# Optimization experiments

Measured on AMD Instinct MI355X. Metric: run time of the kernel, lower is better.

The kernel has to match this reference:

```python
import jax, jax.numpy as jnp
import numpy as np

EPS = 1e-6


def _ring_view(t, start, length, M):
    # contiguous logical view of `length` oldest positions starting at start
    if start + length <= M:
        return t[:, start:start + length]
    first = t[:, start:]
    return jnp.concatenate([first, t[:, :length - first.shape[1]]], axis=1)


def _ring_write(t, start, chunk, M):
    # write chunk at logical position `start`, wrapping around the ring
    C = chunk.shape[1]
    if start + C <= M:
        return t.at[:, start:start + C].set(chunk)
    first = M - start
    t = t.at[:, start:].set(chunk[:, :first])
    return t.at[:, :C - first].set(chunk[:, first:])


def setup_inputs() -> dict:
    key = jax.random.key(0)
    ks = jax.random.split(key, 9)
    B, M, Hh, D, F, C = 4, 1088, 32, 128, 128, 512
    f = lambda k, s: jax.random.normal(k, s, dtype=jnp.float32)
    return {
        "K": f(ks[0], (B, M, Hh, D)),
        "V": f(ks[1], (B, M, Hh, D)),
        "FK": f(ks[2], (B, M, Hh, F)),
        "H": f(ks[3], (B, Hh, F, D)),
        "S": f(ks[4], (B, Hh, F)),
        "k_c": f(ks[5], (B, C, Hh, D)),
        "v_c": f(ks[6], (B, C, Hh, D)),
        "fk_c": f(ks[7], (B, C, Hh, F)),
        "fq": f(ks[8], (B, C, Hh, F)),
        "write_ptr": 100,
        "valid": 1088,
    }


def reference(K, V, FK, H, S, k_c, v_c, fk_c, fq, write_ptr, valid):
    M = K.shape[1]
    C = k_c.shape[1]
    if valid + C <= M:
        # room left in ring buffer: plain write, no eviction
        pos = (write_ptr + valid) % M
        K = _ring_write(K, pos, k_c, M)
        V = _ring_write(V, pos, v_c, M)
        FK = _ring_write(FK, pos, fk_c, M)
    else:
        # evict num_excess oldest tokens into recurrent state H, S
        num_excess = valid + C - M
        old_fk = _ring_view(FK, write_ptr, num_excess, M)  # (B, E, H, F)
        old_v = _ring_view(V, write_ptr, num_excess, M)    # (B, E, H, D)
        H = H + jnp.einsum('behf,behd->bhfd', old_fk, old_v)
        S = S + old_fk.sum(axis=1)
        write_ptr = (write_ptr + num_excess) % M
        pos = (write_ptr + M) % M  # valid == M now
        K = _ring_write(K, pos, k_c, M)
        V = _ring_write(V, pos, v_c, M)
        FK = _ring_write(FK, pos, fk_c, M)
    # linear_attn_forward(fq)
    y_num = jnp.einsum('bchf,bhfd->bchd', fq, H)
    y_den = jnp.einsum('bchf,bhf->bch', fq, S)[..., None]
    return y_num, y_den, K, V, FK, H, S
```

## Files before the change

### kernel.cpp

```cpp
#include <hip/hip_runtime.h>

typedef float f32x4 __attribute__((ext_vector_type(4)));

constexpr int B  = 4;
constexpr int M  = 1088;
constexpr int HH = 32;
constexpr int D  = 128;
constexpr int F  = 128;
constexpr int C  = 512;

constexpr int SZ_YNUM = B * C * HH * D;
constexpr int SZ_YDEN = B * C * HH;
constexpr int SZ_KVM  = B * M * HH * D;
constexpr int SZ_H    = B * HH * F * D;

constexpr int OFF_YNUM = 0;
constexpr int OFF_YDEN = OFF_YNUM + SZ_YNUM;
constexpr int OFF_K    = OFF_YDEN + SZ_YDEN;
constexpr int OFF_V    = OFF_K + SZ_KVM;
constexpr int OFF_FK   = OFF_V + SZ_KVM;
constexpr int OFF_H    = OFF_FK + SZ_KVM;
constexpr int OFF_S    = OFF_H + SZ_H;

constexpr int INNER4      = HH * D / 4;
constexpr int ROWS_PER_CB = 4;
constexpr int COPY_BLOCKS = B * M / ROWS_PER_CB;
constexpr int HS_BLOCKS   = B * HH * 2;
constexpr int Y_BLOCKS    = B * HH * 8;
constexpr int ESTEP       = 16;

__device__ __forceinline__ void ring_params(const int* wp_p, const int* valid_p,
                                            int& wp, int& num_excess, int& pos) {
    wp = *wp_p;
    int valid = *valid_p;
    if (valid + C <= M) {
        num_excess = 0;
        pos = (wp + valid) % M;
    } else {
        num_excess = valid + C - M;
        pos = (wp + num_excess) % M;
    }
}

__device__ __forceinline__ void ring_copy_block(int cb, int tid,
                                                const f32x4* __restrict__ src,
                                                const f32x4* __restrict__ chk,
                                                f32x4* __restrict__ dst,
                                                int pos) {
    int bm0 = cb * ROWS_PER_CB;
#pragma unroll
    for (int r = 0; r < ROWS_PER_CB; ++r) {
        int bm = bm0 + r;
        int m = bm % M;
        int b = bm / M;
        int off = m - pos;
        if (off < 0) off += M;
        const f32x4* s = (off < C) ? &chk[(b * C + off) * INNER4]
                                   : &src[bm * INNER4];
        f32x4* d = &dst[bm * INNER4];
#pragma unroll
        for (int k = 0; k < INNER4 / 256; ++k)
            d[k * 256 + tid] = s[k * 256 + tid];
    }
}

__device__ void update_hs_body(int bx,
                               const float* __restrict__ FKi,
                               const float* __restrict__ Vi,
                               const float* __restrict__ Hi,
                               const float* __restrict__ Si,
                               float* __restrict__ Ho,
                               float* __restrict__ So,
                               int wp, int num_excess) {
    const int tid = threadIdx.x;
    const int fhalf = bx & 1;
    const int bh = bx >> 1;
    const int h = bh & (HH - 1);
    const int b = bh >> 5;
    const int fbase = fhalf * 64;

    __shared__ float  fk_s[ESTEP][64];
    __shared__ f32x4  v_s[ESTEP][32];
    __shared__ float  sred[4][64];

    const int tf = tid >> 5;
    const int td = tid & 31;
    const int cq = tid & 63;
    const int qq = tid >> 6;

    f32x4 acc[8];
#pragma unroll
    for (int i = 0; i < 8; ++i) acc[i] = (f32x4)0.f;
    float s_part = 0.f;

    float fkA[4], fkB[4];
    f32x4 vA[2],  vB[2];

    auto load_tile = [&](int e0, float* fk_r, f32x4* v_r) {
#pragma unroll
        for (int j = 0; j < 4; ++j) {
            int e = e0 + qq + 4 * j;
            int me = wp + e;
            if (me >= M) me -= M;
            if (me >= M) me -= M;
            float v = 0.f;
            if (e < num_excess) v = FKi[((b * M + me) * HH + h) * F + fbase + cq];
            fk_r[j] = v;
        }
#pragma unroll
        for (int j = 0; j < 2; ++j) {
            int e = e0 + tf + 8 * j;
            int me = wp + e;
            if (me >= M) me -= M;
            if (me >= M) me -= M;
            f32x4 v = (f32x4)0.f;
            if (e < num_excess) v = *(const f32x4*)&Vi[((b * M + me) * HH + h) * D + td * 4];
            v_r[j] = v;
        }
    };
    auto store_tile = [&](const float* fk_r, const f32x4* v_r) {
#pragma unroll
        for (int j = 0; j < 4; ++j) fk_s[qq + 4 * j][cq] = fk_r[j];
#pragma unroll
        for (int j = 0; j < 2; ++j) v_s[tf + 8 * j][td] = v_r[j];
    };
    auto compute = [&]() {
#pragma unroll
        for (int ee = 0; ee < ESTEP; ++ee) {
            f32x4 fa = *(const f32x4*)&fk_s[ee][tf * 8];
            f32x4 fb = *(const f32x4*)&fk_s[ee][tf * 8 + 4];
            f32x4 vv = v_s[ee][td];
            acc[0] += fa.x * vv; acc[1] += fa.y * vv;
            acc[2] += fa.z * vv; acc[3] += fa.w * vv;
            acc[4] += fb.x * vv; acc[5] += fb.y * vv;
            acc[6] += fb.z * vv; acc[7] += fb.w * vv;
        }
#pragma unroll
        for (int j = 0; j < 4; ++j) s_part += fk_s[qq * 4 + j][cq];
    };

    if (num_excess > 0) {
        const int nt = (num_excess + ESTEP - 1) / ESTEP;
        load_tile(0, fkA, vA);
        if (nt > 1) load_tile(ESTEP, fkB, vB);
        store_tile(fkA, vA);
        for (int t = 0; t < nt; t += 2) {
            __syncthreads();
            if (t + 2 < nt) load_tile((t + 2) * ESTEP, fkA, vA);
            compute();
            __syncthreads();
            if (t + 1 >= nt) break;
            store_tile(fkB, vB);
            __syncthreads();
            if (t + 3 < nt) load_tile((t + 3) * ESTEP, fkB, vB);
            compute();
            __syncthreads();
            if (t + 2 >= nt) break;
            store_tile(fkA, vA);
        }
    }

    sred[qq][cq] = s_part;
    __syncthreads();
    if (tid < 64) {
        int f = fbase + tid;
        int si = (b * HH + h) * F + f;
        So[si] = Si[si] + sred[0][tid] + sred[1][tid] + sred[2][tid] + sred[3][tid];
    }

#pragma unroll
    for (int i = 0; i < 8; ++i) {
        int f = fbase + tf * 8 + i;
        int base = ((b * HH + h) * F + f) * D + td * 4;
        f32x4 hold = *(const f32x4*)&Hi[base];
        *(f32x4*)&Ho[base] = hold + acc[i];
    }
}

__device__ void compute_y_den_body(int bx,
                                   const float* __restrict__ fq,
                                   const float* __restrict__ Hn,
                                   const float* __restrict__ Sn,
                                   float* __restrict__ ynum,
                                   float* __restrict__ yden) {
    const int tid = threadIdx.x;
    int t0 = bx;
    const int ct = t0 & 7; t0 >>= 3;
    const int h = t0 & (HH - 1);
    const int b = t0 >> 5;
    const int c0 = ct * 64;
    const int bh = b * HH + h;

    __shared__ float  fq_s[32][65];
    __shared__ f32x4  h_s[32][32];
    __shared__ float  S_s[128];
    __shared__ float  den_s[64][4];

    const int tc = tid >> 5;
    const int td = tid & 31;
    const int cq = tid & 63;
    const int qq = tid >> 6;

    if (tid < 128) S_s[tid] = Sn[bh * F + tid];

    f32x4 acc[8];
#pragma unroll
    for (int i = 0; i < 8; ++i) acc[i] = (f32x4)0.f;
    float den_part = 0.f;

    for (int f0 = 0; f0 < F; f0 += 32) {
#pragma unroll
        for (int r = 0; r < 8; ++r) {
            int idx = tid + r * 256;
            int cc = idx >> 5, ee = idx & 31;
            fq_s[ee][cc] = fq[((b * C + c0 + cc) * HH + h) * F + f0 + ee];
        }
#pragma unroll
        for (int r = 0; r < 4; ++r) {
            int idx = tid + r * 256;
            int row = idx >> 5, col = idx & 31;
            h_s[row][col] = *(const f32x4*)&Hn[(bh * F + f0 + row) * D + col * 4];
        }
        __syncthreads();
#pragma unroll
        for (int ee = 0; ee < 32; ++ee) {
            f32x4 hv = h_s[ee][td];
#pragma unroll
            for (int i = 0; i < 8; ++i) {
                float q = fq_s[ee][tc * 8 + i];
                acc[i] += q * hv;
            }
        }
#pragma unroll
        for (int j = 0; j < 8; ++j)
            den_part += fq_s[qq * 8 + j][cq] * S_s[f0 + qq * 8 + j];
        __syncthreads();
    }

    den_s[cq][qq] = den_part;
    __syncthreads();
    if (tid < 64)
        yden[(b * C + c0 + tid) * HH + h] =
            den_s[tid][0] + den_s[tid][1] + den_s[tid][2] + den_s[tid][3];

#pragma unroll
    for (int i = 0; i < 8; ++i) {
        int c = c0 + tc * 8 + i;
        int base = ((b * C + c) * HH + h) * D + td * 4;
        *(f32x4*)&ynum[base] = acc[i];
    }
}

__global__ __launch_bounds__(256) void fused_hs_vfk(
        const float* __restrict__ FKi, const float* __restrict__ Vi,
        const float* __restrict__ Hi,  const float* __restrict__ Si,
        float* __restrict__ Ho,        float* __restrict__ So,
        const f32x4* __restrict__ V4,  const f32x4* __restrict__ vc,  f32x4* __restrict__ oV,
        const f32x4* __restrict__ FK4, const f32x4* __restrict__ fkc, f32x4* __restrict__ oFK,
        const int* __restrict__ wp_p,  const int* __restrict__ valid_p) {
    int wp, num_excess, pos;
    ring_params(wp_p, valid_p, wp, num_excess, pos);

    int bx = blockIdx.x;
    if (bx < HS_BLOCKS) {
        update_hs_body(bx, FKi, Vi, Hi, Si, Ho, So, wp, num_excess);
        return;
    }
    bx -= HS_BLOCKS;
    if (bx < COPY_BLOCKS) {
        ring_copy_block(bx, threadIdx.x, V4, vc, oV, pos);
        return;
    }
    bx -= COPY_BLOCKS;
    ring_copy_block(bx, threadIdx.x, FK4, fkc, oFK, pos);
}

__global__ __launch_bounds__(256) void fused_y_k(
        const float* __restrict__ fq, const float* __restrict__ Hn,
        const float* __restrict__ Sn,
        float* __restrict__ ynum,     float* __restrict__ yden,
        const f32x4* __restrict__ K4, const f32x4* __restrict__ kc,
        f32x4* __restrict__ oK,
        const int* __restrict__ wp_p, const int* __restrict__ valid_p) {
    int wp, num_excess, pos;
    ring_params(wp_p, valid_p, wp, num_excess, pos);

    int bx = blockIdx.x;
    if (bx < Y_BLOCKS) {
        compute_y_den_body(bx, fq, Hn, Sn, ynum, yden);
        return;
    }
    bx -= Y_BLOCKS;
    ring_copy_block(bx, threadIdx.x, K4, kc, oK, pos);
}

extern "C" void kernel_launch(void* const* d_in, const int* in_sizes, int n_in,
                              void* d_out, int out_size, void* d_ws, size_t ws_size,
                              hipStream_t stream) {
    const float* K   = (const float*)d_in[0];
    const float* V   = (const float*)d_in[1];
    const float* FK  = (const float*)d_in[2];
    const float* H   = (const float*)d_in[3];
    const float* S   = (const float*)d_in[4];
    const float* k_c = (const float*)d_in[5];
    const float* v_c = (const float*)d_in[6];
    const float* fk_c= (const float*)d_in[7];
    const float* fq  = (const float*)d_in[8];
    const int* wp    = (const int*)d_in[9];
    const int* valid = (const int*)d_in[10];

    float* out = (float*)d_out;
    float* o_ynum = out + OFF_YNUM;
    float* o_yden = out + OFF_YDEN;
    float* o_K    = out + OFF_K;
    float* o_V    = out + OFF_V;
    float* o_FK   = out + OFF_FK;
    float* o_H    = out + OFF_H;
    float* o_S    = out + OFF_S;

    fused_hs_vfk<<<HS_BLOCKS + 2 * COPY_BLOCKS, 256, 0, stream>>>(
        FK, V, H, S, o_H, o_S,
        (const f32x4*)V,  (const f32x4*)v_c,  (f32x4*)o_V,
        (const f32x4*)FK, (const f32x4*)fk_c, (f32x4*)o_FK,
        wp, valid);

    fused_y_k<<<Y_BLOCKS + COPY_BLOCKS, 256, 0, stream>>>(
        fq, o_H, o_S, o_ynum, o_yden,
        (const f32x4*)K, (const f32x4*)k_c, (f32x4*)o_K,
        wp, valid);
}
```

Baseline: 152.6 us.

## Split fused kernels into separate H/S, Y, and ring-copy launches

Replaces the two fused kernels, which mixed H/S update or Y compute with ring-buffer copy blocks, with three kernels: H/S update, Y computation, and a single 3D-grid copy of K, V and FK. The H/S load loop also changes from double-buffered register tiles to a single register tile that is prefetched before each compute step. The aim is to stop the small compute blocks from being starved or delayed by bandwidth-heavy copy blocks in the same grid, and to lower register pressure. In exchange the copies no longer overlap with the compute stages inside one launch, and there is an extra kernel launch.

```diff
diff --git a/kernel.cpp b/kernel.cpp
--- a/kernel.cpp
+++ b/kernel.cpp
@@ -42,12 +42,21 @@
     }
 }
 
-__device__ __forceinline__ void ring_copy_block(int cb, int tid,
-                                                const f32x4* __restrict__ src,
-                                                const f32x4* __restrict__ chk,
-                                                f32x4* __restrict__ dst,
-                                                int pos) {
-    int bm0 = cb * ROWS_PER_CB;
+__global__ __launch_bounds__(256) void copy3_kernel(
+        const f32x4* __restrict__ K4,  const f32x4* __restrict__ kc,  f32x4* __restrict__ oK,
+        const f32x4* __restrict__ V4,  const f32x4* __restrict__ vc,  f32x4* __restrict__ oV,
+        const f32x4* __restrict__ FK4, const f32x4* __restrict__ fkc, f32x4* __restrict__ oFK,
+        const int* __restrict__ wp_p,  const int* __restrict__ valid_p) {
+    int wp, num_excess, pos;
+    ring_params(wp_p, valid_p, wp, num_excess, pos);
+
+    const int z = blockIdx.z;
+    const f32x4* src = (z == 0) ? K4 : (z == 1) ? V4 : FK4;
+    const f32x4* chk = (z == 0) ? kc : (z == 1) ? vc : fkc;
+    f32x4*       dst = (z == 0) ? oK : (z == 1) ? oV : oFK;
+
+    const int tid = threadIdx.x;
+    int bm0 = blockIdx.x * ROWS_PER_CB;
 #pragma unroll
     for (int r = 0; r < ROWS_PER_CB; ++r) {
         int bm = bm0 + r;
@@ -64,15 +73,16 @@
     }
 }
 
-__device__ void update_hs_body(int bx,
-                               const float* __restrict__ FKi,
-                               const float* __restrict__ Vi,
-                               const float* __restrict__ Hi,
-                               const float* __restrict__ Si,
-                               float* __restrict__ Ho,
-                               float* __restrict__ So,
-                               int wp, int num_excess) {
+__global__ __launch_bounds__(256) void hs_kernel(
+        const float* __restrict__ FKi, const float* __restrict__ Vi,
+        const float* __restrict__ Hi,  const float* __restrict__ Si,
+        float* __restrict__ Ho,        float* __restrict__ So,
+        const int* __restrict__ wp_p,  const int* __restrict__ valid_p) {
+    int wp, num_excess, pos;
+    ring_params(wp_p, valid_p, wp, num_excess, pos);
+
     const int tid = threadIdx.x;
+    const int bx = blockIdx.x;
     const int fhalf = bx & 1;
     const int bh = bx >> 1;
     const int h = bh & (HH - 1);
@@ -93,10 +103,10 @@
     for (int i = 0; i < 8; ++i) acc[i] = (f32x4)0.f;
     float s_part = 0.f;
 
-    float fkA[4], fkB[4];
-    f32x4 vA[2],  vB[2];
-
-    auto load_tile = [&](int e0, float* fk_r, f32x4* v_r) {
+    float fk_r[4];
+    f32x4 v_r[2];
+
+    auto load_tile = [&](int e0) {
 #pragma unroll
         for (int j = 0; j < 4; ++j) {
             int e = e0 + qq + 4 * j;
@@ -118,45 +128,34 @@
             v_r[j] = v;
         }
     };
-    auto store_tile = [&](const float* fk_r, const f32x4* v_r) {
+    auto store_tile = [&]() {
 #pragma unroll
         for (int j = 0; j < 4; ++j) fk_s[qq + 4 * j][cq] = fk_r[j];
 #pragma unroll
         for (int j = 0; j < 2; ++j) v_s[tf + 8 * j][td] = v_r[j];
     };
-    auto compute = [&]() {
-#pragma unroll
-        for (int ee = 0; ee < ESTEP; ++ee) {
-            f32x4 fa = *(const f32x4*)&fk_s[ee][tf * 8];
-            f32x4 fb = *(const f32x4*)&fk_s[ee][tf * 8 + 4];
-            f32x4 vv = v_s[ee][td];
-            acc[0] += fa.x * vv; acc[1] += fa.y * vv;
-            acc[2] += fa.z * vv; acc[3] += fa.w * vv;
-            acc[4] += fb.x * vv; acc[5] += fb.y * vv;
-            acc[6] += fb.z * vv; acc[7] += fb.w * vv;
-        }
-#pragma unroll
-        for (int j = 0; j < 4; ++j) s_part += fk_s[qq * 4 + j][cq];
-    };
 
     if (num_excess > 0) {
-        const int nt = (num_excess + ESTEP - 1) / ESTEP;
-        load_tile(0, fkA, vA);
-        if (nt > 1) load_tile(ESTEP, fkB, vB);
-        store_tile(fkA, vA);
-        for (int t = 0; t < nt; t += 2) {
+        load_tile(0);
+        store_tile();
+        for (int e0 = 0; e0 < num_excess; e0 += ESTEP) {
+            bool more = (e0 + ESTEP < num_excess);
+            if (more) load_tile(e0 + ESTEP);
             __syncthreads();
-            if (t + 2 < nt) load_tile((t + 2) * ESTEP, fkA, vA);
-            compute();
+#pragma unroll
+            for (int ee = 0; ee < ESTEP; ++ee) {
+                f32x4 fa = *(const f32x4*)&fk_s[ee][tf * 8];
+                f32x4 fb = *(const f32x4*)&fk_s[ee][tf * 8 + 4];
+                f32x4 vv = v_s[ee][td];
+                acc[0] += fa.x * vv; acc[1] += fa.y * vv;
+                acc[2] += fa.z * vv; acc[3] += fa.w * vv;
+                acc[4] += fb.x * vv; acc[5] += fb.y * vv;
+                acc[6] += fb.z * vv; acc[7] += fb.w * vv;
+            }
+#pragma unroll
+            for (int j = 0; j < 4; ++j) s_part += fk_s[qq * 4 + j][cq];
             __syncthreads();
-            if (t + 1 >= nt) break;
-            store_tile(fkB, vB);
-            __syncthreads();
-            if (t + 3 < nt) load_tile((t + 3) * ESTEP, fkB, vB);
-            compute();
-            __syncthreads();
-            if (t + 2 >= nt) break;
-            store_tile(fkA, vA);
+            if (more) store_tile();
         }
     }
 
@@ -177,14 +176,12 @@
     }
 }
 
-__device__ void compute_y_den_body(int bx,
-                                   const float* __restrict__ fq,
-                                   const float* __restrict__ Hn,
-                                   const float* __restrict__ Sn,
-                                   float* __restrict__ ynum,
-                                   float* __restrict__ yden) {
+__global__ __launch_bounds__(256) void y_kernel(
+        const float* __restrict__ fq, const float* __restrict__ Hn,
+        const float* __restrict__ Sn,
+        float* __restrict__ ynum,     float* __restrict__ yden) {
     const int tid = threadIdx.x;
-    int t0 = bx;
+    int t0 = blockIdx.x;
     const int ct = t0 & 7; t0 >>= 3;
     const int h = t0 & (HH - 1);
     const int b = t0 >> 5;
@@ -249,49 +246,6 @@
         int base = ((b * C + c) * HH + h) * D + td * 4;
         *(f32x4*)&ynum[base] = acc[i];
     }
-}
-
-__global__ __launch_bounds__(256) void fused_hs_vfk(
-        const float* __restrict__ FKi, const float* __restrict__ Vi,
-        const float* __restrict__ Hi,  const float* __restrict__ Si,
-        float* __restrict__ Ho,        float* __restrict__ So,
-        const f32x4* __restrict__ V4,  const f32x4* __restrict__ vc,  f32x4* __restrict__ oV,
-        const f32x4* __restrict__ FK4, const f32x4* __restrict__ fkc, f32x4* __restrict__ oFK,
-        const int* __restrict__ wp_p,  const int* __restrict__ valid_p) {
-    int wp, num_excess, pos;
-    ring_params(wp_p, valid_p, wp, num_excess, pos);
-
-    int bx = blockIdx.x;
-    if (bx < HS_BLOCKS) {
-        update_hs_body(bx, FKi, Vi, Hi, Si, Ho, So, wp, num_excess);
-        return;
-    }
-    bx -= HS_BLOCKS;
-    if (bx < COPY_BLOCKS) {
-        ring_copy_block(bx, threadIdx.x, V4, vc, oV, pos);
-        return;
-    }
-    bx -= COPY_BLOCKS;
-    ring_copy_block(bx, threadIdx.x, FK4, fkc, oFK, pos);
-}
-
-__global__ __launch_bounds__(256) void fused_y_k(
-        const float* __restrict__ fq, const float* __restrict__ Hn,
-        const float* __restrict__ Sn,
-        float* __restrict__ ynum,     float* __restrict__ yden,
-        const f32x4* __restrict__ K4, const f32x4* __restrict__ kc,
-        f32x4* __restrict__ oK,
-        const int* __restrict__ wp_p, const int* __restrict__ valid_p) {
-    int wp, num_excess, pos;
-    ring_params(wp_p, valid_p, wp, num_excess, pos);
-
-    int bx = blockIdx.x;
-    if (bx < Y_BLOCKS) {
-        compute_y_den_body(bx, fq, Hn, Sn, ynum, yden);
-        return;
-    }
-    bx -= Y_BLOCKS;
-    ring_copy_block(bx, threadIdx.x, K4, kc, oK, pos);
 }
 
 extern "C" void kernel_launch(void* const* d_in, const int* in_sizes, int n_in,
@@ -318,14 +272,13 @@
     float* o_H    = out + OFF_H;
     float* o_S    = out + OFF_S;
 
-    fused_hs_vfk<<<HS_BLOCKS + 2 * COPY_BLOCKS, 256, 0, stream>>>(
-        FK, V, H, S, o_H, o_S,
+    hs_kernel<<<HS_BLOCKS, 256, 0, stream>>>(FK, V, H, S, o_H, o_S, wp, valid);
+
+    y_kernel<<<Y_BLOCKS, 256, 0, stream>>>(fq, o_H, o_S, o_ynum, o_yden);
+
+    copy3_kernel<<<dim3(COPY_BLOCKS, 1, 3), 256, 0, stream>>>(
+        (const f32x4*)K,  (const f32x4*)k_c,  (f32x4*)o_K,
         (const f32x4*)V,  (const f32x4*)v_c,  (f32x4*)o_V,
         (const f32x4*)FK, (const f32x4*)fk_c, (f32x4*)o_FK,
         wp, valid);
-
-    fused_y_k<<<Y_BLOCKS + COPY_BLOCKS, 256, 0, stream>>>(
-        fq, o_H, o_S, o_ynum, o_yden,
-        (const f32x4*)K, (const f32x4*)k_c, (f32x4*)o_K,
-        wp, valid);
-}
+}
```

New measurement: 219.6 us. 1.44x slower.
